# Kernel optimization log

Hardware: AMD Instinct MI355X
Metric: run time of the kernel (lower is better)

## Reference

```python
import jax, jax.numpy as jnp
import numpy as np

B, T, I, H = 64, 512, 256, 1024


def setup_inputs() -> dict:
    key = jax.random.key(0)
    ks = jax.random.split(key, 20)
    stdv = float(1.0 / np.sqrt(H))
    u = lambda k, shape: jax.random.uniform(k, shape, jnp.float32, -stdv, stdv)
    d = {
        "inputs": jax.random.normal(ks[0], (B, T, I), jnp.float32),
        "h0": jax.random.normal(ks[1], (1, B, H), jnp.float32),
        "c0": jax.random.normal(ks[2], (1, B, H), jnp.float32),
    }
    names = ["w_ii", "w_hi", "b_ii", "b_hi",
             "w_if", "w_hf", "b_if", "b_hf",
             "w_io", "w_ho", "b_io", "b_ho",
             "w_ig", "w_hg", "b_ig", "b_hg"]
    shapes = {"w_i": (H, I), "w_h": (H, H), "b_i": (H,), "b_h": (H,)}
    for j, n in enumerate(names):
        d[n] = u(ks[3 + j], shapes[n[:3]])
    return d


def reference(inputs, h0, c0,
              w_ii, w_hi, b_ii, b_hi,
              w_if, w_hf, b_if, b_hf,
              w_io, w_ho, b_io, b_ho,
              w_ig, w_hg, b_ig, b_hg):
    # Fuse the 4 gate GEMMs into one: gate order i, f, g, o.
    Wx = jnp.concatenate([w_ii, w_if, w_ig, w_io], axis=0)  # (4H, I)
    Wh = jnp.concatenate([w_hi, w_hf, w_hg, w_ho], axis=0)  # (4H, H)
    b = jnp.concatenate([b_ii + b_hi, b_if + b_hf, b_ig + b_hg, b_io + b_ho], axis=0)  # (4H,)
    # Precompute all input projections in one big GEMM: (T, B, 4H)
    x_proj = jnp.einsum('bti,gi->tbg', inputs, Wx) + b

    def step(carry, xp):
        h, c = carry                       # (B, H), (B, H)
        z = xp + h @ Wh.T                  # (B, 4H)
        i = jax.nn.sigmoid(z[:, :H])
        f = jax.nn.sigmoid(z[:, H:2 * H])
        g = jnp.tanh(z[:, 2 * H:3 * H])
        o = jax.nn.sigmoid(z[:, 3 * H:])
        c = f * c + i * g
        h = o * jnp.tanh(c)
        return (h, c), h

    (h, c), hs = jax.lax.scan(step, (h0[0], c0[0]), x_proj)
    hidden_seq = jnp.transpose(hs, (1, 0, 2))  # (B, T, H)
    return hidden_seq, (h[None], c[None])
```

## Files before the change

### kernel.cpp

```cpp
#include <hip/hip_runtime.h>
#include <hip/hip_bf16.h>

#define TT 512
#define BB 64
#define II 256
#define HH 1024
#define NWG 256
#define MB 16
#define NJ 16
#define NR 64
#define KTOT 1280
#define WU 120
#define WROWB 1920
#define HROWB 2048
#define FPAD 16
#define MAXTRY (1 << 20)

typedef __bf16 bf16x8 __attribute__((ext_vector_type(8)));
typedef float f32x4 __attribute__((ext_vector_type(4)));
typedef unsigned uint32x4 __attribute__((ext_vector_type(4)));
typedef unsigned uint32x2 __attribute__((ext_vector_type(2)));

__device__ inline uint32x4 ld16_sc1(const void* p) {
  uint32x4 r;
  asm volatile("global_load_dwordx4 %0, %1, off sc1" : "=&v"(r) : "v"(p));
  return r;
}


__global__ __launch_bounds__(256) void k_cast_inputs(const float* __restrict__ in,
                                                     __hip_bfloat16* __restrict__ outp) {
  int i = (blockIdx.x * 256 + threadIdx.x) * 4;
  float4 v = *reinterpret_cast<const float4*>(in + i);
  outp[i + 0] = __float2bfloat16(v.x);
  outp[i + 1] = __float2bfloat16(v.y);
  outp[i + 2] = __float2bfloat16(v.z);
  outp[i + 3] = __float2bfloat16(v.w);
}

__global__ __launch_bounds__(256) void k_pack_w(
    const float* __restrict__ wxi, const float* __restrict__ whi,
    const float* __restrict__ wxf, const float* __restrict__ whf,
    const float* __restrict__ wxg, const float* __restrict__ whg,
    const float* __restrict__ wxo, const float* __restrict__ who,
    __hip_bfloat16* __restrict__ Wp) {
  int t = blockIdx.x * 256 + threadIdx.x;
  int p = t / 320;
  int k4 = (t - p * 320) * 4;
  int j = p >> 2, gate = p & 3;
  const float* wx = (gate == 0) ? wxi : (gate == 1) ? wxf : (gate == 2) ? wxg : wxo;
  const float* wh = (gate == 0) ? whi : (gate == 1) ? whf : (gate == 2) ? whg : who;
  float4 v;
  if (k4 < II) v = *reinterpret_cast<const float4*>(wx + (size_t)j * II + k4);
  else         v = *reinterpret_cast<const float4*>(wh + (size_t)j * HH + (k4 - II));
  __hip_bfloat16* o = Wp + (size_t)p * KTOT + k4;
  o[0] = __float2bfloat16(v.x);
  o[1] = __float2bfloat16(v.y);
  o[2] = __float2bfloat16(v.z);
  o[3] = __float2bfloat16(v.w);
}

__global__ __launch_bounds__(256) void k_pack_bias_h0(
    const float* __restrict__ bii, const float* __restrict__ bhi,
    const float* __restrict__ bif, const float* __restrict__ bhf,
    const float* __restrict__ bg,  const float* __restrict__ bhg,
    const float* __restrict__ bio, const float* __restrict__ bho,
    const float* __restrict__ h0, float* __restrict__ biasp,
    __hip_bfloat16* __restrict__ hb, unsigned* __restrict__ flags) {
  int i = blockIdx.x * 256 + threadIdx.x;
  if (i < 4096) {
    int j = i >> 2, gate = i & 3;
    const float* bi = (gate == 0) ? bii : (gate == 1) ? bif : (gate == 2) ? bg : bio;
    const float* bh = (gate == 0) ? bhi : (gate == 1) ? bhf : (gate == 2) ? bhg : bho;
    biasp[i] = bi[j] + bh[j];
    flags[i] = 0;
  }
  hb[i] = __float2bfloat16(h0[i]);
}


__global__ __launch_bounds__(256, 1) void k_lstm(
    const __hip_bfloat16* __restrict__ xb,
    const __hip_bfloat16* __restrict__ Wp,
    const float* __restrict__ biasp,
    const float* __restrict__ c0,
    __hip_bfloat16* __restrict__ hbuf,
    unsigned* __restrict__ flags,
    float* __restrict__ out)
{
  extern __shared__ __align__(16) char smem[];
  char* Wl = smem;
  char* Hs = smem + 122880;
  char* Zx = smem + 155648;
  char* Ho = smem + 160768;

  const int tid = threadIdx.x;
  const int lane = tid & 63;
  const int wq = tid >> 6;
  const int bt = blockIdx.x >> 6;
  const int gt = blockIdx.x & 63;
  const int b0 = bt * MB;
  const int r0 = gt * NR;

  const int l15 = lane & 15;
  const int kqu = lane >> 4;

  {
    const int u = tid & 127;
    const bool act = u < WU;
    uint32x4 wtmp[16];
#pragma unroll
    for (int q = 0; q < 16; ++q) {
      int row = q * 2 + (tid >> 7);
      if (act) wtmp[q] = *reinterpret_cast<const uint32x4*>(
          Wp + (size_t)(r0 + row) * KTOT + II + u * 8);
    }
#pragma unroll
    for (int q = 0; q < 16; ++q) {
      int row = q * 2 + (tid >> 7);
      if (act) *reinterpret_cast<uint32x4*>(Wl + row * WROWB + ((u ^ (row & 7)) << 4)) = wtmp[q];
    }
#pragma unroll
    for (int q = 0; q < 16; ++q) {
      int row = 32 + q * 2 + (tid >> 7);
      if (act) wtmp[q] = *reinterpret_cast<const uint32x4*>(
          Wp + (size_t)(r0 + row) * KTOT + II + u * 8);
    }
#pragma unroll
    for (int q = 0; q < 16; ++q) {
      int row = 32 + q * 2 + (tid >> 7);
      if (act) *reinterpret_cast<uint32x4*>(Wl + row * WROWB + ((u ^ (row & 7)) << 4)) = wtmp[q];
    }
  }

  const int brow = r0 + wq * 16 + l15;
  bf16x8 wxr[8], wht0, wht1;
  {
    const __hip_bfloat16* ws = Wp + (size_t)brow * KTOT + kqu * 8;
#pragma unroll
    for (int kk = 0; kk < 8; ++kk)
      wxr[kk] = *reinterpret_cast<const bf16x8*>(ws + kk * 32);
    wht0 = *reinterpret_cast<const bf16x8*>(ws + II + 960);
    wht1 = *reinterpret_cast<const bf16x8*>(ws + II + 992);
  }

  const int m_e = 4 * kqu + (lane & 3);
  const int tq = (lane >> 2) & 3;
  const int j_g = gt * NJ + wq * 4 + tq;
  const int b_g = b0 + m_e;
  const float4 bias = *reinterpret_cast<const float4*>(biasp + j_g * 4);
  float c_reg = c0[(size_t)b_g * HH + j_g];

  const int hs_swz = l15 & 7;
  const int bn_row = wq * 16 + l15;
  const int bn_swz = bn_row & 7;
  char* ZxW = Zx + wq * 1280;
  char* HoW = Ho + wq * 128;

  {
    uint32x4 tmp[8];
#pragma unroll
    for (int q = 0; q < 8; ++q) {
      int idx = q * 64 + lane;
      int rl = wq * 4 + (idx >> 7);
      int u = idx & 127;
      tmp[q] = ld16_sc1(hbuf + (size_t)(b0 + rl) * HH + u * 8);
    }
    asm volatile("s_waitcnt vmcnt(0)" ::: "memory");
    __builtin_amdgcn_sched_barrier(0);
#pragma unroll
    for (int q = 0; q < 8; ++q) {
      int idx = q * 64 + lane;
      int rl = wq * 4 + (idx >> 7);
      int u = idx & 127;
      *reinterpret_cast<uint32x4*>(Hs + rl * HROWB + ((u ^ (rl & 7)) << 4)) = tmp[q];
    }
  }

  const __hip_bfloat16* xrowA = xb + (size_t)(b0 + l15) * (TT * II) + kqu * 8;
  f32x4 accs[4];
#pragma unroll
  for (int q = 0; q < 4; ++q) accs[q] = (f32x4){0.f, 0.f, 0.f, 0.f};
#pragma unroll
  for (int kk = 0; kk < 8; ++kk) {
    bf16x8 xa = *reinterpret_cast<const bf16x8*>(xrowA + kk * 32);
    accs[kk & 3] = __builtin_amdgcn_mfma_f32_16x16x32_bf16(xa, wxr[kk], accs[kk & 3], 0, 0, 0);
  }

  __syncthreads();

  for (int t = 0; t < TT; ++t) {
#pragma unroll
    for (int kk = 0; kk < 30; ++kk) {
      int u = kk * 4 + kqu;
      bf16x8 a = *reinterpret_cast<const bf16x8*>(Hs + l15 * HROWB + ((u ^ hs_swz) << 4));
      bf16x8 b = *reinterpret_cast<const bf16x8*>(Wl + bn_row * WROWB + ((u ^ bn_swz) << 4));
      accs[kk & 3] = __builtin_amdgcn_mfma_f32_16x16x32_bf16(a, b, accs[kk & 3], 0, 0, 0);
    }
    {
      int u = 120 + kqu;
      bf16x8 a = *reinterpret_cast<const bf16x8*>(Hs + l15 * HROWB + ((u ^ hs_swz) << 4));
      accs[2] = __builtin_amdgcn_mfma_f32_16x16x32_bf16(a, wht0, accs[2], 0, 0, 0);
    }
    {
      int u = 124 + kqu;
      bf16x8 a = *reinterpret_cast<const bf16x8*>(Hs + l15 * HROWB + ((u ^ hs_swz) << 4));
      accs[3] = __builtin_amdgcn_mfma_f32_16x16x32_bf16(a, wht1, accs[3], 0, 0, 0);
    }
    f32x4 acc = (accs[0] + accs[1]) + (accs[2] + accs[3]);

    *reinterpret_cast<f32x4*>(ZxW + l15 * 80 + kqu * 16) = acc;
    asm volatile("s_waitcnt lgkmcnt(0)" ::: "memory");
    __builtin_amdgcn_sched_barrier(0);
    float zi = *reinterpret_cast<const float*>(ZxW + (4 * tq + 0) * 80 + m_e * 4) + bias.x;
    float zf = *reinterpret_cast<const float*>(ZxW + (4 * tq + 1) * 80 + m_e * 4) + bias.y;
    float zg = *reinterpret_cast<const float*>(ZxW + (4 * tq + 2) * 80 + m_e * 4) + bias.z;
    float zo = *reinterpret_cast<const float*>(ZxW + (4 * tq + 3) * 80 + m_e * 4) + bias.w;

    float ig = 1.f / (1.f + __expf(-zi));
    float fg = 1.f / (1.f + __expf(-zf));
    float gg = 2.f / (1.f + __expf(-2.f * zg)) - 1.f;
    float og = 1.f / (1.f + __expf(-zo));
    c_reg = fg * c_reg + ig * gg;
    float tc = 2.f / (1.f + __expf(-2.f * c_reg)) - 1.f;
    float h = og * tc;

    if (t == TT - 1) {
      out[(size_t)b_g * (TT * HH) + (size_t)t * HH + j_g] = h;
      out[(size_t)BB * TT * HH + (size_t)b_g * HH + j_g] = h;
      out[(size_t)BB * TT * HH + BB * HH + (size_t)b_g * HH + j_g] = c_reg;
      break;
    }

    __hip_bfloat16 hb16 = __float2bfloat16(h);
    *reinterpret_cast<unsigned short*>(HoW + m_e * 8 + tq * 2) =
        *reinterpret_cast<unsigned short*>(&hb16);
    asm volatile("s_waitcnt lgkmcnt(0)" ::: "memory");
    __builtin_amdgcn_sched_barrier(0);

    const int nxt = (t + 1) & 1;
    const unsigned gen = (unsigned)(t + 1);
    if (lane < 16) {
      uint32x2 hv = *reinterpret_cast<const uint32x2*>(HoW + lane * 8);
      __hip_bfloat16* dst = hbuf + (size_t)nxt * (BB * HH)
                          + (size_t)(b0 + lane) * HH + gt * NJ + wq * 4;
      asm volatile("global_store_dwordx2 %0, %1, off sc1" :: "v"(dst), "v"(hv) : "memory");
    }
    asm volatile("s_waitcnt vmcnt(0)" ::: "memory");

    __syncthreads();

    if (tid == 0) {
      asm volatile("global_store_dword %0, %1, off sc1"
                   :: "v"(flags + (bt * 64 + gt) * FPAD), "v"(gen) : "memory");
    }

    out[(size_t)b_g * (TT * HH) + (size_t)t * HH + j_g] = h;
#pragma unroll
    for (int q = 0; q < 4; ++q) accs[q] = (f32x4){0.f, 0.f, 0.f, 0.f};
    {
      const __hip_bfloat16* xp = xrowA + (size_t)(t + 1) * II;
#pragma unroll
      for (int kk = 0; kk < 8; ++kk) {
        bf16x8 xa = *reinterpret_cast<const bf16x8*>(xp + kk * 32);
        accs[kk & 3] = __builtin_amdgcn_mfma_f32_16x16x32_bf16(xa, wxr[kk], accs[kk & 3], 0, 0, 0);
      }
    }

    if (wq == 0) {
      const unsigned* fp = flags + (bt * 64 + lane) * FPAD;
      int tries = 0;
      unsigned f;
      for (;;) {
        asm volatile("global_load_dword %0, %1, off sc1\n\ts_waitcnt vmcnt(0)"
                     : "=&v"(f) : "v"(fp) : "memory");
        if (__all(f >= gen) || ++tries > MAXTRY) break;
      }
    }
    __syncthreads();

    {
      uint32x4 tmp[8];
      const __hip_bfloat16* hsrc = hbuf + (size_t)nxt * (BB * HH);
#pragma unroll
      for (int q = 0; q < 8; ++q) {
        int idx = q * 64 + lane;
        int rl = wq * 4 + (idx >> 7);
        int u = idx & 127;
        tmp[q] = ld16_sc1(hsrc + (size_t)(b0 + rl) * HH + u * 8);
      }
      asm volatile("s_waitcnt vmcnt(0)" ::: "memory");
      __builtin_amdgcn_sched_barrier(0);
#pragma unroll
      for (int q = 0; q < 8; ++q) {
        int idx = q * 64 + lane;
        int rl = wq * 4 + (idx >> 7);
        int u = idx & 127;
        *reinterpret_cast<uint32x4*>(Hs + rl * HROWB + ((u ^ (rl & 7)) << 4)) = tmp[q];
      }
    }
    __syncthreads();
  }
}


extern "C" void kernel_launch(void* const* d_in, const int* in_sizes, int n_in,
                              void* d_out, int out_size, void* d_ws, size_t ws_size,
                              hipStream_t stream) {
  (void)in_sizes; (void)n_in; (void)out_size; (void)ws_size;
  const float* inputs = (const float*)d_in[0];
  const float* h0 = (const float*)d_in[1];
  const float* c0 = (const float*)d_in[2];
  const float* w_ii = (const float*)d_in[3];
  const float* w_hi = (const float*)d_in[4];
  const float* b_ii = (const float*)d_in[5];
  const float* b_hi = (const float*)d_in[6];
  const float* w_if = (const float*)d_in[7];
  const float* w_hf = (const float*)d_in[8];
  const float* b_if = (const float*)d_in[9];
  const float* b_hf = (const float*)d_in[10];
  const float* w_io = (const float*)d_in[11];
  const float* w_ho = (const float*)d_in[12];
  const float* b_io = (const float*)d_in[13];
  const float* b_ho = (const float*)d_in[14];
  const float* w_ig = (const float*)d_in[15];
  const float* w_hg = (const float*)d_in[16];
  const float* b_ig = (const float*)d_in[17];
  const float* b_hg = (const float*)d_in[18];

  char* ws = (char*)d_ws;
  __hip_bfloat16* xb    = (__hip_bfloat16*)ws;
  __hip_bfloat16* Wp    = (__hip_bfloat16*)(ws + 16777216);
  float*          biasp = (float*)(ws + 27262976);
  __hip_bfloat16* hbuf  = (__hip_bfloat16*)(ws + 27279360);
  unsigned*       flags = (unsigned*)(ws + 27541504);
  float* out = (float*)d_out;

  k_cast_inputs<<<8192, 256, 0, stream>>>(inputs, xb);
  k_pack_w<<<5120, 256, 0, stream>>>(w_ii, w_hi, w_if, w_hf, w_ig, w_hg, w_io, w_ho, Wp);
  k_pack_bias_h0<<<256, 256, 0, stream>>>(b_ii, b_hi, b_if, b_hf, b_ig, b_hg,
                                          b_io, b_ho, h0, biasp, hbuf, flags);

  const int lds_bytes = 161280;
  hipFuncSetAttribute((const void*)k_lstm,
                      hipFuncAttributeMaxDynamicSharedMemorySize, lds_bytes);
  void* args[] = {(void*)&xb, (void*)&Wp, (void*)&biasp, (void*)&c0,
                  (void*)&hbuf, (void*)&flags, (void*)&out};
  hipError_t e = hipLaunchCooperativeKernel((void*)k_lstm, dim3(NWG), dim3(256),
                                            args, lds_bytes, stream);
  if (e != hipSuccess) {
    k_lstm<<<dim3(NWG), dim3(256), lds_bytes, stream>>>(xb, Wp, biasp, c0, hbuf, flags, out);
  }
}
```

Before: 2.281 ms.

## Use per-wave flags and split H reload to overlap recurrent MFMA with loads

Each wave now stores its own h values directly as bf16 shorts and publishes a per-wave flag, so the LDS staging of h and two block-wide barriers per step go away. Every wave polls the flags of its batch group with dwordx4 loads instead of one wave polling followed by a syncthreads. The next-step h reload is split into two halves, so the first 16 k-chunks of the recurrent GEMM run while the second half of the global loads is still arriving. The cost is more, smaller global stores and more polling traffic across waves, and ordering now relies on per-wave store and flag visibility.

```diff
diff --git a/kernel.cpp b/kernel.cpp
--- a/kernel.cpp
+++ b/kernel.cpp
@@ -13,13 +13,12 @@
 #define WU 120
 #define WROWB 1920
 #define HROWB 2048
-#define FPAD 16
+#define NFLAG 1024
 #define MAXTRY (1 << 20)
 
 typedef __bf16 bf16x8 __attribute__((ext_vector_type(8)));
 typedef float f32x4 __attribute__((ext_vector_type(4)));
 typedef unsigned uint32x4 __attribute__((ext_vector_type(4)));
-typedef unsigned uint32x2 __attribute__((ext_vector_type(2)));
 
 __device__ inline uint32x4 ld16_sc1(const void* p) {
   uint32x4 r;
@@ -73,8 +72,8 @@
     const float* bi = (gate == 0) ? bii : (gate == 1) ? bif : (gate == 2) ? bg : bio;
     const float* bh = (gate == 0) ? bhi : (gate == 1) ? bhf : (gate == 2) ? bhg : bho;
     biasp[i] = bi[j] + bh[j];
-    flags[i] = 0;
-  }
+  }
+  if (i < NFLAG) flags[i] = 0;
   hb[i] = __float2bfloat16(h0[i]);
 }
 
@@ -92,7 +91,6 @@
   char* Wl = smem;
   char* Hs = smem + 122880;
   char* Zx = smem + 155648;
-  char* Ho = smem + 160768;
 
   const int tid = threadIdx.x;
   const int lane = tid & 63;
@@ -155,24 +153,21 @@
   const int bn_row = wq * 16 + l15;
   const int bn_swz = bn_row & 7;
   char* ZxW = Zx + wq * 1280;
-  char* HoW = Ho + wq * 128;
 
   {
     uint32x4 tmp[8];
 #pragma unroll
     for (int q = 0; q < 8; ++q) {
-      int idx = q * 64 + lane;
-      int rl = wq * 4 + (idx >> 7);
-      int u = idx & 127;
+      int rl = wq * 4 + (q & 3);
+      int u = (q >> 2) * 64 + lane;
       tmp[q] = ld16_sc1(hbuf + (size_t)(b0 + rl) * HH + u * 8);
     }
     asm volatile("s_waitcnt vmcnt(0)" ::: "memory");
     __builtin_amdgcn_sched_barrier(0);
 #pragma unroll
     for (int q = 0; q < 8; ++q) {
-      int idx = q * 64 + lane;
-      int rl = wq * 4 + (idx >> 7);
-      int u = idx & 127;
+      int rl = wq * 4 + (q & 3);
+      int u = (q >> 2) * 64 + lane;
       *reinterpret_cast<uint32x4*>(Hs + rl * HROWB + ((u ^ (rl & 7)) << 4)) = tmp[q];
     }
   }
@@ -189,9 +184,17 @@
 
   __syncthreads();
 
+#pragma unroll
+  for (int kk = 0; kk < 16; ++kk) {
+    int u = kk * 4 + kqu;
+    bf16x8 a = *reinterpret_cast<const bf16x8*>(Hs + l15 * HROWB + ((u ^ hs_swz) << 4));
+    bf16x8 b = *reinterpret_cast<const bf16x8*>(Wl + bn_row * WROWB + ((u ^ bn_swz) << 4));
+    accs[kk & 3] = __builtin_amdgcn_mfma_f32_16x16x32_bf16(a, b, accs[kk & 3], 0, 0, 0);
+  }
+
   for (int t = 0; t < TT; ++t) {
 #pragma unroll
-    for (int kk = 0; kk < 30; ++kk) {
+    for (int kk = 16; kk < 30; ++kk) {
       int u = kk * 4 + kqu;
       bf16x8 a = *reinterpret_cast<const bf16x8*>(Hs + l15 * HROWB + ((u ^ hs_swz) << 4));
       bf16x8 b = *reinterpret_cast<const bf16x8*>(Wl + bn_row * WROWB + ((u ^ bn_swz) << 4));
@@ -232,27 +235,13 @@
       break;
     }
 
-    __hip_bfloat16 hb16 = __float2bfloat16(h);
-    *reinterpret_cast<unsigned short*>(HoW + m_e * 8 + tq * 2) =
-        *reinterpret_cast<unsigned short*>(&hb16);
-    asm volatile("s_waitcnt lgkmcnt(0)" ::: "memory");
-    __builtin_amdgcn_sched_barrier(0);
-
     const int nxt = (t + 1) & 1;
     const unsigned gen = (unsigned)(t + 1);
-    if (lane < 16) {
-      uint32x2 hv = *reinterpret_cast<const uint32x2*>(HoW + lane * 8);
-      __hip_bfloat16* dst = hbuf + (size_t)nxt * (BB * HH)
-                          + (size_t)(b0 + lane) * HH + gt * NJ + wq * 4;
-      asm volatile("global_store_dwordx2 %0, %1, off sc1" :: "v"(dst), "v"(hv) : "memory");
-    }
-    asm volatile("s_waitcnt vmcnt(0)" ::: "memory");
-
-    __syncthreads();
-
-    if (tid == 0) {
-      asm volatile("global_store_dword %0, %1, off sc1"
-                   :: "v"(flags + (bt * 64 + gt) * FPAD), "v"(gen) : "memory");
+    {
+      __hip_bfloat16 hb16 = __float2bfloat16(h);
+      unsigned hv = (unsigned)*reinterpret_cast<unsigned short*>(&hb16);
+      __hip_bfloat16* dst = hbuf + (size_t)nxt * (BB * HH) + (size_t)b_g * HH + j_g;
+      asm volatile("global_store_short %0, %1, off sc1" :: "v"(dst), "v"(hv) : "memory");
     }
 
     out[(size_t)b_g * (TT * HH) + (size_t)t * HH + j_g] = h;
@@ -266,40 +255,61 @@
         accs[kk & 3] = __builtin_amdgcn_mfma_f32_16x16x32_bf16(xa, wxr[kk], accs[kk & 3], 0, 0, 0);
       }
     }
-
-    if (wq == 0) {
-      const unsigned* fp = flags + (bt * 64 + lane) * FPAD;
+    asm volatile("s_waitcnt vmcnt(0)" ::: "memory");
+    if (lane == 0) {
+      asm volatile("global_store_dword %0, %1, off sc1"
+                   :: "v"(flags + bt * 256 + gt * 4 + wq), "v"(gen) : "memory");
+    }
+
+    {
+      const unsigned* fp = flags + bt * 256 + lane * 4;
       int tries = 0;
-      unsigned f;
+      uint32x4 f;
       for (;;) {
-        asm volatile("global_load_dword %0, %1, off sc1\n\ts_waitcnt vmcnt(0)"
+        asm volatile("global_load_dwordx4 %0, %1, off sc1\n\ts_waitcnt vmcnt(0)"
                      : "=&v"(f) : "v"(fp) : "memory");
-        if (__all(f >= gen) || ++tries > MAXTRY) break;
-      }
-    }
-    __syncthreads();
+        int ok = (f.x >= gen) && (f.y >= gen) && (f.z >= gen) && (f.w >= gen);
+        if (__all(ok) || ++tries > MAXTRY) break;
+      }
+    }
 
     {
       uint32x4 tmp[8];
       const __hip_bfloat16* hsrc = hbuf + (size_t)nxt * (BB * HH);
 #pragma unroll
       for (int q = 0; q < 8; ++q) {
-        int idx = q * 64 + lane;
-        int rl = wq * 4 + (idx >> 7);
-        int u = idx & 127;
+        int rl = wq * 4 + (q & 3);
+        int u = (q >> 2) * 64 + lane;
         tmp[q] = ld16_sc1(hsrc + (size_t)(b0 + rl) * HH + u * 8);
       }
+      asm volatile("s_waitcnt vmcnt(4)" ::: "memory");
+      __builtin_amdgcn_sched_barrier(0);
+#pragma unroll
+      for (int q = 0; q < 4; ++q) {
+        int rl = wq * 4 + q;
+        *reinterpret_cast<uint32x4*>(Hs + rl * HROWB + ((lane ^ (rl & 7)) << 4)) = tmp[q];
+      }
+      asm volatile("s_waitcnt lgkmcnt(0)" ::: "memory");
+      __builtin_amdgcn_s_barrier();
+
+#pragma unroll
+      for (int kk = 0; kk < 16; ++kk) {
+        int u = kk * 4 + kqu;
+        bf16x8 a = *reinterpret_cast<const bf16x8*>(Hs + l15 * HROWB + ((u ^ hs_swz) << 4));
+        bf16x8 b = *reinterpret_cast<const bf16x8*>(Wl + bn_row * WROWB + ((u ^ bn_swz) << 4));
+        accs[kk & 3] = __builtin_amdgcn_mfma_f32_16x16x32_bf16(a, b, accs[kk & 3], 0, 0, 0);
+      }
+
       asm volatile("s_waitcnt vmcnt(0)" ::: "memory");
       __builtin_amdgcn_sched_barrier(0);
 #pragma unroll
-      for (int q = 0; q < 8; ++q) {
-        int idx = q * 64 + lane;
-        int rl = wq * 4 + (idx >> 7);
-        int u = idx & 127;
-        *reinterpret_cast<uint32x4*>(Hs + rl * HROWB + ((u ^ (rl & 7)) << 4)) = tmp[q];
-      }
-    }
-    __syncthreads();
+      for (int q = 4; q < 8; ++q) {
+        int rl = wq * 4 + (q & 3);
+        *reinterpret_cast<uint32x4*>(Hs + rl * HROWB + (((64 + lane) ^ (rl & 7)) << 4)) = tmp[q];
+      }
+      asm volatile("s_waitcnt lgkmcnt(0)" ::: "memory");
+      __builtin_amdgcn_s_barrier();
+    }
   }
 }
 
@@ -341,7 +351,7 @@
   k_pack_bias_h0<<<256, 256, 0, stream>>>(b_ii, b_hi, b_if, b_hf, b_ig, b_hg,
                                           b_io, b_ho, h0, biasp, hbuf, flags);
 
-  const int lds_bytes = 161280;
+  const int lds_bytes = 160768;
   hipFuncSetAttribute((const void*)k_lstm,
                       hipFuncAttributeMaxDynamicSharedMemorySize, lds_bytes);
   void* args[] = {(void*)&xb, (void*)&Wp, (void*)&biasp, (void*)&c0,
```

Measured after the change: 5.108 ms. 124% more time.
